# Kernel tuning notes

Measured on AMD Instinct MI355X. Metric: run time of the kernel, lower is better.

Reference implementation:

```python
import jax, jax.numpy as jnp
import numpy as np
from jax import lax

B, C, H, W = 16, 256, 64, 64  # inplanes=256, planes=2*inplanes=512


def ste_sign(x):
    # forward: sign(x); backward: clipped straight-through (|x|<=1)
    c = jnp.clip(x, -1.0, 1.0)
    return c + lax.stop_gradient(jnp.sign(x) - c)


def conv_ada(x, w, ka, kw):
    # 1-bit activations scaled by learnable scalar ka
    a_b = ste_sign(x) * ka
    # 1-bit weights with per-out-channel XNOR-style scale * learnable kw
    alpha = jnp.mean(jnp.abs(w), axis=(1, 2, 3), keepdims=True) * kw  # [O,1,1,1]
    w_b = ste_sign(w) * alpha
    return lax.conv_general_dilated(a_b, w_b, window_strides=(1, 1),
                                    padding=((1, 1), (1, 1)),
                                    dimension_numbers=('NCHW', 'OIHW', 'NCHW'))


def prelu(x, slope):
    s = slope.reshape(1, -1, 1, 1)
    return jnp.where(x >= 0, x, s * x)


def pixel_unshuffle2(x):
    b, c, h, w = x.shape
    x = x.reshape(b, c, h // 2, 2, w // 2, 2)
    x = x.transpose(0, 1, 3, 5, 2, 4)  # (b, c, r1, r2, h2, w2)
    return x.reshape(b, c * 4, h // 2, w // 2)


def setup_inputs() -> dict:
    key = jax.random.key(0)
    ks = jax.random.split(key, 8)
    inp = {
        'x': jax.random.normal(ks[0], (B, C, H, W), dtype=jnp.float32),
        'conv1_w': jax.random.normal(ks[1], (C, C, 3, 3), dtype=jnp.float32) * 0.05,
        'conv2_w': jax.random.normal(ks[2], (C // 2, C, 3, 3), dtype=jnp.float32) * 0.05,
        'bias1_': jnp.zeros((1, C, 1, 1), jnp.float32),
        'bias1': jnp.zeros((1, C, 1, 1), jnp.float32),
        'bias2': jnp.zeros((1, C, 1, 1), jnp.float32),
        'bias2_': jnp.zeros((1, C, 1, 1), jnp.float32),
        'bias3': jnp.zeros((1, C // 2, 1, 1), jnp.float32),
        'bias4': jnp.zeros((1, C // 2, 1, 1), jnp.float32),
        'ka1': jnp.asarray(1.0, jnp.float32),
        'kw1': jnp.asarray(0.2, jnp.float32),
        'ka2': jnp.asarray(1.0, jnp.float32),
        'kw2': jnp.asarray(0.2, jnp.float32),
        'prelu1_w': jnp.full((C,), 0.25, jnp.float32),
        'prelu2_w': jnp.full((C // 2,), 0.25, jnp.float32),
    }
    return inp


def reference(x, conv1_w, conv2_w, bias1_, bias1, bias2, bias2_, bias3, bias4,
              ka1, kw1, ka2, kw2, prelu1_w, prelu2_w):
    out = x + bias1_                      # move1_
    out = conv_ada(out, conv1_w, ka1, kw1)  # conv1
    xres = out + x                        # residual add
    # NOTE: in the original forward, move1/prelu1/move2 output is overwritten
    # (dead branch); kept here for faithfulness but it does not affect output.
    _dead = prelu(out + bias1, prelu1_w) + bias2
    out = xres + bias2_                   # move2_
    out = conv_ada(out, conv2_w, ka2, kw2)  # conv2 -> C//2 channels
    shortcut = xres[:, :xres.shape[1] // 2, :, :]
    out = out + shortcut
    out = out + bias3                     # move3
    out = prelu(out, prelu2_w)            # prelu2
    out = out + bias4                     # move4
    out = pixel_unshuffle2(out)           # -> [B, 2*C, H/2, W/2]
    return out
```

## Files before the change

### kernel.cpp

```cpp
#include <hip/hip_runtime.h>
#include <hip/hip_bf16.h>
#include <stdint.h>

#define B_   16
#define C_   256
#define H_   64
#define W_   64
#define PH   66
#define PW   66
#define K1   2304
#define NO1  256
#define NO2  128

typedef signed char i8;
typedef int   int32x4 __attribute__((ext_vector_type(4)));

__device__ __forceinline__ void gl_lds16(const void* src, void* dst) {
    __builtin_amdgcn_global_load_lds(
        (const __attribute__((address_space(1))) unsigned int*)src,
        (__attribute__((address_space(3))) unsigned int*)dst, 16, 0, 0);
}

__device__ __forceinline__ i8 sign_i8(float v) {
    return (v > 0.f) ? (i8)1 : ((v < 0.f) ? (i8)(-1) : (i8)0);
}

__global__ void halo_zero(i8* __restrict__ s1, i8* __restrict__ s2) {
    int t = blockIdx.x * blockDim.x + threadIdx.x;
    const int total = B_ * PH * PW * (C_ / 16);
    if (t >= total) return;
    int pix = t >> 4;
    int c16 = t & 15;
    int pw  = pix % PW;
    int ph  = (pix / PW) % PH;
    if (ph != 0 && ph != PH - 1 && pw != 0 && pw != PW - 1) return;
    int4 z = make_int4(0, 0, 0, 0);
    *(int4*)(s1 + (size_t)pix * C_ + c16 * 16) = z;
    *(int4*)(s2 + (size_t)pix * C_ + c16 * 16) = z;
}

__global__ void prep_s1(const float* __restrict__ x, const float* __restrict__ bias1_,
                        i8* __restrict__ s1) {
    __shared__ i8 tile[64][272];
    int b = blockIdx.x >> 6;
    int h = blockIdx.x & 63;
    int t = threadIdx.x;
    int w  = t & 63;
    int cq = t >> 6;
    for (int i = 0; i < 64; ++i) {
        int c = cq * 64 + i;
        float v = x[((size_t)(b * C_ + c) * H_ + h) * W_ + w] + bias1_[c];
        tile[w][c] = sign_i8(v);
    }
    __syncthreads();
    for (int i = 0; i < 4; ++i) {
        int idx = i * 256 + t;
        int w2  = idx >> 4;
        int cb  = (idx & 15) * 16;
        int4 v = *(const int4*)&tile[w2][cb];
        *(int4*)(s1 + ((size_t)(b * PH + h + 1) * PW + (w2 + 1)) * C_ + cb) = v;
    }
}

__global__ void prep_w(const float* __restrict__ w1, const float* __restrict__ w2,
                       const float* __restrict__ ka1, const float* __restrict__ kw1,
                       const float* __restrict__ ka2, const float* __restrict__ kw2,
                       i8* __restrict__ Bt1, i8* __restrict__ Bt2,
                       float* __restrict__ scale1, float* __restrict__ scale2) {
    int o = blockIdx.x;
    const float* w; i8* Bt; float* scale; float kk;
    if (o < NO1) { w = w1 + (size_t)o * K1;         Bt = Bt1 + (size_t)o * K1;         scale = scale1 + o;         kk = ka1[0] * kw1[0]; }
    else         { int oo = o - NO1;
                   w = w2 + (size_t)oo * K1;        Bt = Bt2 + (size_t)oo * K1;        scale = scale2 + oo;        kk = ka2[0] * kw2[0]; }
    int t = threadIdx.x;
    float s = 0.f;
    for (int e = t; e < K1; e += 256) {
        float v = w[e];
        s += fabsf(v);
        int c = e / 9, tap = e % 9;
        Bt[tap * 256 + c] = sign_i8(v);
    }
    for (int off = 32; off; off >>= 1) s += __shfl_down(s, off);
    __shared__ float red[4];
    if ((t & 63) == 0) red[t >> 6] = s;
    __syncthreads();
    if (t == 0) {
        float tot = red[0] + red[1] + red[2] + red[3];
        *scale = kk * tot * (1.0f / 2304.0f);
    }
}

template<int EPI>
__device__ __forceinline__ void conv_body(
               char* lds,
               const i8* __restrict__ Sin, const i8* __restrict__ Bt,
               const float* __restrict__ scale,
               const float* __restrict__ xaux,
               const float* __restrict__ biasA,
               const float* __restrict__ bias4,
               const float* __restrict__ slope,
               i8*   __restrict__ s2out,
               float* __restrict__ xres_out,
               float* __restrict__ dout)
{
    char* Alds = lds;
    char* Bs0  = lds + 101376;
    char* Bs1  = Bs0 + 16384;
    char* Bs2  = Bs1 + 16384;

    int t  = threadIdx.x;

    int wg    = blockIdx.x;
    int chunk = gridDim.x >> 3;
    int logical = (wg & 7) * chunk + (wg >> 3);
    int nb, mb;
    if (EPI == 1) { nb = logical & 1; mb = logical >> 1; }
    else          { nb = 0;           mb = logical; }
    int b  = mb >> 4;
    int h0 = (mb & 15) * 4;

    int l  = t & 63;
    int wv = t >> 6;
    int wr = wv >> 1;
    int wc = wv & 1;

    int br0  = t >> 3;
    int bsrc = ((t & 7) * 16) ^ (((t >> 3) & 7) << 4);
    int blin = (t & 7) * 16;

    auto stageB = [&](int ks, char* Bs) {
        int tap = ks >> 1;
        int c0  = (ks & 1) * 128;
#pragma unroll
        for (int i = 0; i < 2; ++i) {
            int r = br0 + i * 64;
            int n = nb * 128 + r;
            const i8* gb = Bt + (size_t)n * K1 + tap * 256 + c0 + bsrc;
            gl_lds16(gb, Bs + r * 128 + blin);
        }
    };

    stageB(0, Bs0);
    stageB(1, Bs1);
    for (int i = 0; i < 13; ++i) {
        int idx = i * 512 + t;
        if (idx < 6336) {
            int r6   = idx / 1056;
            int rem  = idx - r6 * 1056;
            int w66  = rem >> 4;
            int slot = rem & 15;
            int pix  = r6 * 66 + w66;
            const i8* ga = Sin + ((size_t)(b * PH + h0 + r6) * PW + w66) * 256
                               + ((slot ^ (pix & 7)) << 4);
            gl_lds16(ga, Alds + idx * 16);
        }
    }
    asm volatile("s_waitcnt vmcnt(0)" ::: "memory");
    __builtin_amdgcn_s_barrier();

    int q = l >> 4;
    int pixbase[4];
#pragma unroll
    for (int mi = 0; mi < 4; ++mi) {
        int m = wr * 64 + mi * 16 + (l & 15);
        pixbase[mi] = (m >> 6) * 66 + (m & 63);
    }
    int rx = (l & 7) << 4;
    int bfbase[4];
#pragma unroll
    for (int ni = 0; ni < 4; ++ni)
        bfbase[ni] = (wc * 64 + ni * 16 + (l & 15)) * 128;
    int bfoff[2] = { (q * 16) ^ rx, (64 + q * 16) ^ rx };

    int32x4 acc[4][4];
#pragma unroll
    for (int mi = 0; mi < 4; ++mi)
#pragma unroll
        for (int ni = 0; ni < 4; ++ni) acc[mi][ni] = (int32x4){0, 0, 0, 0};

    char* pr = Bs0; char* pn = Bs1; char* ps = Bs2;

    for (int ks = 0; ks < 18; ++ks) {
        if (ks < 16) stageB(ks + 2, ps);
        {
            int tap  = ks >> 1;
            int toff = (tap / 3) * 66 + (tap % 3);
            int c8   = (ks & 1) << 7;
            __builtin_amdgcn_s_setprio(1);
#pragma unroll
            for (int kk = 0; kk < 2; ++kk) {
                int qk = kk * 4 + q;
                int32x4 af[4], bf[4];
#pragma unroll
                for (int mi = 0; mi < 4; ++mi) {
                    int pixm = pixbase[mi] + toff;
                    int addr = pixm * 256 + c8 + ((qk ^ (pixm & 7)) << 4);
                    af[mi] = *(const int32x4*)(Alds + addr);
                }
#pragma unroll
                for (int ni = 0; ni < 4; ++ni)
                    bf[ni] = *(const int32x4*)(pr + bfbase[ni] + bfoff[kk]);
#pragma unroll
                for (int mi = 0; mi < 4; ++mi)
#pragma unroll
                    for (int ni = 0; ni < 4; ++ni)
                        acc[mi][ni] = __builtin_amdgcn_mfma_i32_16x16x64_i8(af[mi], bf[ni], acc[mi][ni], 0, 0, 0);
            }
            __builtin_amdgcn_s_setprio(0);
        }
        if (ks < 16)      asm volatile("s_waitcnt vmcnt(2)" ::: "memory");
        else if (ks == 16) asm volatile("s_waitcnt vmcnt(0)" ::: "memory");
        if (ks < 17) __builtin_amdgcn_s_barrier();
        char* tmp = pr; pr = pn; pn = ps; ps = tmp;
    }

    int co = l & 15;
    int ro = l >> 4;
#pragma unroll
    for (int mi = 0; mi < 4; ++mi) {
#pragma unroll
        for (int ni = 0; ni < 4; ++ni) {
            int n_loc = wc * 64 + ni * 16 + co;
            int o = nb * 128 + n_loc;
            float sc = scale[o];
#pragma unroll
            for (int j = 0; j < 4; ++j) {
                int m_loc = wr * 64 + mi * 16 + ro * 4 + j;
                int h = h0 + (m_loc >> 6);
                int w = m_loc & 63;
                float v = (float)acc[mi][ni][j] * sc;
                if (EPI == 1) {
                    float xv = xaux[((size_t)(b * C_ + o) * H_ + h) * W_ + w];
                    float xr = v + xv;
                    float sv = xr + biasA[o];
                    s2out[((size_t)(b * PH + h + 1) * PW + (w + 1)) * C_ + o] = sign_i8(sv);
                    if (o < NO2)
                        xres_out[(((size_t)b * H_ + h) * W_ + w) * NO2 + o] = xr;
                } else {
                    float xr = xaux[(((size_t)b * H_ + h) * W_ + w) * NO2 + o];
                    float vv = v + xr + biasA[o];
                    vv = (vv >= 0.f) ? vv : vv * slope[o];
                    vv += bias4[o];
                    int p = h & 1, qq = w & 1;
                    dout[(((size_t)b * 512 + (o * 4 + p * 2 + qq)) * 32 + (h >> 1)) * 32 + (w >> 1)] = vv;
                }
            }
        }
    }
}

__global__ __launch_bounds__(512) void conv_g1(
    const i8* Sin, const i8* Bt, const float* scale, const float* xaux,
    const float* biasA, const float* bias4, const float* slope,
    i8* s2out, float* xres_out, float* dout) {
    extern __shared__ char lds[];
    conv_body<1>(lds, Sin, Bt, scale, xaux, biasA, bias4, slope, s2out, xres_out, dout);
}
__global__ __launch_bounds__(512) void conv_g2(
    const i8* Sin, const i8* Bt, const float* scale, const float* xaux,
    const float* biasA, const float* bias4, const float* slope,
    i8* s2out, float* xres_out, float* dout) {
    extern __shared__ char lds[];
    conv_body<2>(lds, Sin, Bt, scale, xaux, biasA, bias4, slope, s2out, xres_out, dout);
}

static const size_t SZ_S   = (size_t)B_ * PH * PW * C_;
static const size_t OFF_S1 = 0;
static const size_t OFF_S2 = OFF_S1 + SZ_S;
static const size_t OFF_B1 = OFF_S2 + SZ_S;
static const size_t OFF_B2 = OFF_B1 + (size_t)NO1 * K1;
static const size_t OFF_C1 = OFF_B2 + (size_t)NO2 * K1;
static const size_t OFF_C2 = OFF_C1 + 1024;
static const size_t OFF_XR = OFF_C2 + 512;

static const int LDS_BYTES = 101376 + 3 * 16384;

extern "C" void kernel_launch(void* const* d_in, const int* in_sizes, int n_in,
                              void* d_out, int out_size, void* d_ws, size_t ws_size,
                              hipStream_t stream) {
    (void)in_sizes; (void)n_in; (void)out_size; (void)ws_size;
    const float* x      = (const float*)d_in[0];
    const float* w1     = (const float*)d_in[1];
    const float* w2     = (const float*)d_in[2];
    const float* bias1_ = (const float*)d_in[3];
    const float* bias2_ = (const float*)d_in[6];
    const float* bias3  = (const float*)d_in[7];
    const float* bias4  = (const float*)d_in[8];
    const float* ka1    = (const float*)d_in[9];
    const float* kw1    = (const float*)d_in[10];
    const float* ka2    = (const float*)d_in[11];
    const float* kw2    = (const float*)d_in[12];
    const float* slope2 = (const float*)d_in[14];

    char* ws = (char*)d_ws;
    i8*    s1   = (i8*)(ws + OFF_S1);
    i8*    s2   = (i8*)(ws + OFF_S2);
    i8*    Bt1  = (i8*)(ws + OFF_B1);
    i8*    Bt2  = (i8*)(ws + OFF_B2);
    float* sc1  = (float*)(ws + OFF_C1);
    float* sc2  = (float*)(ws + OFF_C2);
    float* xres = (float*)(ws + OFF_XR);
    float* out  = (float*)d_out;

    {
        int total = B_ * PH * PW * (C_ / 16);
        hipLaunchKernelGGL(halo_zero, dim3((total + 255) / 256), dim3(256), 0, stream, s1, s2);
    }
    hipLaunchKernelGGL(prep_s1, dim3(B_ * H_), dim3(256), 0, stream, x, bias1_, s1);
    hipLaunchKernelGGL(prep_w, dim3(NO1 + NO2), dim3(256), 0, stream,
                       w1, w2, ka1, kw1, ka2, kw2, Bt1, Bt2, sc1, sc2);
    hipLaunchKernelGGL(conv_g1, dim3(512), dim3(512), LDS_BYTES, stream,
                       s1, Bt1, sc1, x, bias2_, nullptr, nullptr, s2, xres, nullptr);
    hipLaunchKernelGGL(conv_g2, dim3(256), dim3(512), LDS_BYTES, stream,
                       s2, Bt2, sc2, xres, bias3, bias4, slope2, nullptr, nullptr, out);
}
```

Baseline: 266.8 us.

## Load conv weights directly into registers and fold halo zeroing into prep

The conv kernels no longer stage weight tiles through a triple-buffered LDS ring with barriers. Each lane now loads its B fragments straight from global memory into registers, double-buffered across k-steps, which removes the per-step barriers and cuts LDS use to the activation tile only. Separately, the halo_zero kernel is removed and prep_s1 writes the zero border for both padded buffers, saving a launch and a full-grid pass. The risk is higher global/L2 traffic for weights, since each wave loads them redundantly, plus more register pressure from the two sets of B fragments.

```diff
diff --git a/kernel.cpp b/kernel.cpp
--- a/kernel.cpp
+++ b/kernel.cpp
@@ -25,22 +25,8 @@
     return (v > 0.f) ? (i8)1 : ((v < 0.f) ? (i8)(-1) : (i8)0);
 }
 
-__global__ void halo_zero(i8* __restrict__ s1, i8* __restrict__ s2) {
-    int t = blockIdx.x * blockDim.x + threadIdx.x;
-    const int total = B_ * PH * PW * (C_ / 16);
-    if (t >= total) return;
-    int pix = t >> 4;
-    int c16 = t & 15;
-    int pw  = pix % PW;
-    int ph  = (pix / PW) % PH;
-    if (ph != 0 && ph != PH - 1 && pw != 0 && pw != PW - 1) return;
-    int4 z = make_int4(0, 0, 0, 0);
-    *(int4*)(s1 + (size_t)pix * C_ + c16 * 16) = z;
-    *(int4*)(s2 + (size_t)pix * C_ + c16 * 16) = z;
-}
-
 __global__ void prep_s1(const float* __restrict__ x, const float* __restrict__ bias1_,
-                        i8* __restrict__ s1) {
+                        i8* __restrict__ s1, i8* __restrict__ s2) {
     __shared__ i8 tile[64][272];
     int b = blockIdx.x >> 6;
     int h = blockIdx.x & 63;
@@ -59,6 +45,25 @@
         int cb  = (idx & 15) * 16;
         int4 v = *(const int4*)&tile[w2][cb];
         *(int4*)(s1 + ((size_t)(b * PH + h + 1) * PW + (w2 + 1)) * C_ + cb) = v;
+    }
+    int4 z = make_int4(0, 0, 0, 0);
+    if (t < 64) {
+        int which = t >> 4;
+        int c16   = t & 15;
+        i8* base  = (which < 2) ? s1 : s2;
+        int col   = (which & 1) ? 65 : 0;
+        *(int4*)(base + ((size_t)(b * PH + h + 1) * PW + col) * C_ + c16 * 16) = z;
+    }
+    if (h == 0 || h == 63) {
+        int prow = (h == 0) ? 0 : 65;
+        for (int i = 0; i < 9; ++i) {
+            int idx = i * 256 + t;
+            if (idx < 2112) {
+                i8* base = (idx < 1056) ? s1 : s2;
+                int k    = (idx < 1056) ? idx : idx - 1056;
+                *(int4*)(base + ((size_t)(b * PH + prow) * PW) * C_ + k * 16) = z;
+            }
+        }
     }
 }
 
@@ -92,7 +97,7 @@
 
 template<int EPI>
 __device__ __forceinline__ void conv_body(
-               char* lds,
+               char* Alds,
                const i8* __restrict__ Sin, const i8* __restrict__ Bt,
                const float* __restrict__ scale,
                const float* __restrict__ xaux,
@@ -103,11 +108,6 @@
                float* __restrict__ xres_out,
                float* __restrict__ dout)
 {
-    char* Alds = lds;
-    char* Bs0  = lds + 101376;
-    char* Bs1  = Bs0 + 16384;
-    char* Bs2  = Bs1 + 16384;
-
     int t  = threadIdx.x;
 
     int wg    = blockIdx.x;
@@ -123,25 +123,8 @@
     int wv = t >> 6;
     int wr = wv >> 1;
     int wc = wv & 1;
-
-    int br0  = t >> 3;
-    int bsrc = ((t & 7) * 16) ^ (((t >> 3) & 7) << 4);
-    int blin = (t & 7) * 16;
-
-    auto stageB = [&](int ks, char* Bs) {
-        int tap = ks >> 1;
-        int c0  = (ks & 1) * 128;
-#pragma unroll
-        for (int i = 0; i < 2; ++i) {
-            int r = br0 + i * 64;
-            int n = nb * 128 + r;
-            const i8* gb = Bt + (size_t)n * K1 + tap * 256 + c0 + bsrc;
-            gl_lds16(gb, Bs + r * 128 + blin);
-        }
-    };
-
-    stageB(0, Bs0);
-    stageB(1, Bs1);
+    int q  = l >> 4;
+
     for (int i = 0; i < 13; ++i) {
         int idx = i * 512 + t;
         if (idx < 6336) {
@@ -158,19 +141,18 @@
     asm volatile("s_waitcnt vmcnt(0)" ::: "memory");
     __builtin_amdgcn_s_barrier();
 
-    int q = l >> 4;
     int pixbase[4];
 #pragma unroll
     for (int mi = 0; mi < 4; ++mi) {
         int m = wr * 64 + mi * 16 + (l & 15);
         pixbase[mi] = (m >> 6) * 66 + (m & 63);
     }
-    int rx = (l & 7) << 4;
-    int bfbase[4];
-#pragma unroll
-    for (int ni = 0; ni < 4; ++ni)
-        bfbase[ni] = (wc * 64 + ni * 16 + (l & 15)) * 128;
-    int bfoff[2] = { (q * 16) ^ rx, (64 + q * 16) ^ rx };
+    const i8* bptr[4];
+#pragma unroll
+    for (int ni = 0; ni < 4; ++ni) {
+        int n = nb * 128 + wc * 64 + ni * 16 + (l & 15);
+        bptr[ni] = Bt + (size_t)n * K1 + q * 16;
+    }
 
     int32x4 acc[4][4];
 #pragma unroll
@@ -178,40 +160,43 @@
 #pragma unroll
         for (int ni = 0; ni < 4; ++ni) acc[mi][ni] = (int32x4){0, 0, 0, 0};
 
-    char* pr = Bs0; char* pn = Bs1; char* ps = Bs2;
-
-    for (int ks = 0; ks < 18; ++ks) {
-        if (ks < 16) stageB(ks + 2, ps);
-        {
-            int tap  = ks >> 1;
-            int toff = (tap / 3) * 66 + (tap % 3);
-            int c8   = (ks & 1) << 7;
-            __builtin_amdgcn_s_setprio(1);
-#pragma unroll
-            for (int kk = 0; kk < 2; ++kk) {
-                int qk = kk * 4 + q;
-                int32x4 af[4], bf[4];
-#pragma unroll
-                for (int mi = 0; mi < 4; ++mi) {
-                    int pixm = pixbase[mi] + toff;
-                    int addr = pixm * 256 + c8 + ((qk ^ (pixm & 7)) << 4);
-                    af[mi] = *(const int32x4*)(Alds + addr);
-                }
+    auto loadB = [&](int ks, int32x4 (&dst)[8]) {
+#pragma unroll
+        for (int ni = 0; ni < 4; ++ni) {
+            dst[ni * 2 + 0] = *(const int32x4*)(bptr[ni] + ks * 128);
+            dst[ni * 2 + 1] = *(const int32x4*)(bptr[ni] + ks * 128 + 64);
+        }
+    };
+
+    auto step = [&](int ks, const int32x4 (&bfr)[8]) {
+        int tap  = ks >> 1;
+        int toff = (tap / 3) * 66 + (tap % 3);
+        int c8   = (ks & 1) << 7;
+#pragma unroll
+        for (int kk = 0; kk < 2; ++kk) {
+            int qk = kk * 4 + q;
+            int32x4 af[4];
+#pragma unroll
+            for (int mi = 0; mi < 4; ++mi) {
+                int pixm = pixbase[mi] + toff;
+                af[mi] = *(const int32x4*)(Alds + pixm * 256 + c8 + ((qk ^ (pixm & 7)) << 4));
+            }
+#pragma unroll
+            for (int mi = 0; mi < 4; ++mi)
 #pragma unroll
                 for (int ni = 0; ni < 4; ++ni)
-                    bf[ni] = *(const int32x4*)(pr + bfbase[ni] + bfoff[kk]);
-#pragma unroll
-                for (int mi = 0; mi < 4; ++mi)
-#pragma unroll
-                    for (int ni = 0; ni < 4; ++ni)
-                        acc[mi][ni] = __builtin_amdgcn_mfma_i32_16x16x64_i8(af[mi], bf[ni], acc[mi][ni], 0, 0, 0);
-            }
-            __builtin_amdgcn_s_setprio(0);
-        }
-        if (ks < 16)      asm volatile("s_waitcnt vmcnt(2)" ::: "memory");
-        else if (ks == 16) asm volatile("s_waitcnt vmcnt(0)" ::: "memory");
-        if (ks < 17) __builtin_amdgcn_s_barrier();
-        char* tmp = pr; pr = pn; pn = ps; ps = tmp;
+                    acc[mi][ni] = __builtin_amdgcn_mfma_i32_16x16x64_i8(af[mi], bfr[ni * 2 + kk], acc[mi][ni], 0, 0, 0);
+        }
+    };
+
+    int32x4 bA[8], bB[8];
+    loadB(0, bA);
+#pragma unroll
+    for (int ks2 = 0; ks2 < 9; ++ks2) {
+        loadB(2 * ks2 + 1, bB);
+        step(2 * ks2, bA);
+        if (ks2 < 8) loadB(2 * ks2 + 2, bA);
+        step(2 * ks2 + 1, bB);
     }
 
     int co = l & 15;
@@ -273,7 +258,7 @@
 static const size_t OFF_C2 = OFF_C1 + 1024;
 static const size_t OFF_XR = OFF_C2 + 512;
 
-static const int LDS_BYTES = 101376 + 3 * 16384;
+static const int LDS_BYTES = 101376;
 
 extern "C" void kernel_launch(void* const* d_in, const int* in_sizes, int n_in,
                               void* d_out, int out_size, void* d_ws, size_t ws_size,
@@ -302,11 +287,7 @@
     float* xres = (float*)(ws + OFF_XR);
     float* out  = (float*)d_out;
 
-    {
-        int total = B_ * PH * PW * (C_ / 16);
-        hipLaunchKernelGGL(halo_zero, dim3((total + 255) / 256), dim3(256), 0, stream, s1, s2);
-    }
-    hipLaunchKernelGGL(prep_s1, dim3(B_ * H_), dim3(256), 0, stream, x, bias1_, s1);
+    hipLaunchKernelGGL(prep_s1, dim3(B_ * H_), dim3(256), 0, stream, x, bias1_, s1, s2);
     hipLaunchKernelGGL(prep_w, dim3(NO1 + NO2), dim3(256), 0, stream,
                        w1, w2, ka1, kw1, ka2, kw2, Bt1, Bt2, sc1, sc2);
     hipLaunchKernelGGL(conv_g1, dim3(512), dim3(512), LDS_BYTES, stream,
```

New measurement: 312.8 us. +17.3%, slower.
